# Kernel tuning notes

Hardware: AMD Instinct MI355X
Metric: run time of the kernel (lower is better)

## Reference

```python
import jax, jax.numpy as jnp
import numpy as np

N = 100_000      # nodes
E = 3_200_000    # edges
H = 32           # hidden_dim
L = 4            # num_layers
G = 1_000        # graphs in batch
F_IN = 1         # num_features
C = 2            # num_classes
BN_EPS = 1e-5


def setup_inputs() -> dict:
    key = jax.random.key(0)
    ks = jax.random.split(key, 8)
    s = 0.1  # param init scale
    x = jax.random.normal(ks[0], (N, F_IN), jnp.float32)
    edge_index = jax.random.randint(ks[1], (2, E), 0, N, dtype=jnp.int64)
    batch = jnp.sort(jax.random.randint(ks[2], (N,), 0, G, dtype=jnp.int64))
    return {
        "x": x,
        "edge_index": edge_index,
        "batch": batch,
        "W_enc": jax.random.normal(ks[3], (F_IN, H), jnp.float32) * s,
        "b_enc": jnp.zeros((H,), jnp.float32),
        "eps": jnp.zeros((L,), jnp.float32),           # GIN train_eps, init 0
        "W1": jax.random.normal(ks[4], (L, H, H), jnp.float32) * s,
        "b1": jnp.zeros((L, H), jnp.float32),
        "W2": jax.random.normal(ks[5], (L, H, H), jnp.float32) * s,
        "b2": jnp.zeros((L, H), jnp.float32),
        "gamma": jnp.ones((L, H), jnp.float32),
        "beta": jnp.zeros((L, H), jnp.float32),
        "W_cls": jax.random.normal(ks[6], (H, C), jnp.float32) * s,
        "b_cls": jnp.zeros((C,), jnp.float32),
    }


def reference(x, edge_index, batch, W_enc, b_enc, eps, W1, b1, W2, b2,
              gamma, beta, W_cls, b_cls):
    h = x @ W_enc + b_enc                      # [N, H] node encoder
    src, dst = edge_index[0], edge_index[1]    # message flow src -> dst
    for l in range(L):
        # GINConv: (1+eps)*x + sum_{j in N(i)} x_j
        agg = jax.ops.segment_sum(h[src], dst, num_segments=N)   # [N, H]
        z = (1.0 + eps[l]) * h + agg
        # 2-layer MLP
        z = jnp.maximum(z @ W1[l] + b1[l], 0.0) @ W2[l] + b2[l]
        # BatchNorm1d (training-mode batch statistics over nodes)
        mu = z.mean(axis=0)
        var = z.var(axis=0)
        z = gamma[l] * (z - mu) * jax.lax.rsqrt(var + BN_EPS) + beta[l]
        h = jnp.maximum(z, 0.0)                # ReLU (dropout = identity, eval)
    pooled = jax.ops.segment_sum(h, batch, num_segments=G)   # global_add_pool
    return pooled @ W_cls + b_cls              # [G, C]
```

## Files before the change

kernel.cpp:

```cpp
#include <hip/hip_runtime.h>

#define N_NODES 100000
#define N_EDGES 3200000
#define HD      32
#define NLAYERS 4
#define NGRAPHS 1000
#define BN_EPS  1e-5f
#define BSHIFT  9
#define NBUCK   ((N_NODES + 511) >> 9)
#define PCHUNK  8192
#define NPB     ((N_EDGES + PCHUNK - 1) / PCHUNK)
#define ENC_BLOCKS ((N_NODES * 8 + 255) / 256)

typedef _Float16 f16;
typedef _Float16 f16x8 __attribute__((ext_vector_type(8)));
typedef float    f32x4 __attribute__((ext_vector_type(4)));
typedef int      i32x4 __attribute__((ext_vector_type(4)));
typedef unsigned int  u32x2 __attribute__((ext_vector_type(2)));
typedef unsigned char uc4 __attribute__((ext_vector_type(4)));
typedef unsigned char uc8 __attribute__((ext_vector_type(8)));

__global__ __launch_bounds__(256) void k_encphist(
    const float* __restrict__ x, const float* __restrict__ W_enc,
    const float* __restrict__ b_enc, const int* __restrict__ ei,
    unsigned char* __restrict__ hq, float* __restrict__ stats,
    float* __restrict__ pooled, int* __restrict__ pcnt)
{
    __shared__ int hist[256];
    int bb = blockIdx.x, t = threadIdx.x;
    if (bb < NPB) {
        hist[t] = 0;
        __syncthreads();
        int base4 = bb * (PCHUNK / 4);
        int n4 = min(PCHUNK / 4, N_EDGES / 4 - base4);
        const i32x4* d4 = (const i32x4*)(ei + N_EDGES);
        for (int k = t; k < n4; k += 256) {
            i32x4 d = __builtin_nontemporal_load(d4 + base4 + k);
            atomicAdd(&hist[d.x >> BSHIFT], 1);
            atomicAdd(&hist[d.y >> BSHIFT], 1);
            atomicAdd(&hist[d.z >> BSHIFT], 1);
            atomicAdd(&hist[d.w >> BSHIFT], 1);
        }
        __syncthreads();
        pcnt[t * NPB + bb] = hist[t];
    } else {
        int gid = (bb - NPB) * 256 + t;
        if (gid < NLAYERS * 64)   stats[gid]  = 0.f;
        if (gid < NGRAPHS * HD)   pooled[gid] = 0.f;
        if (gid < N_NODES * 8) {
            int i = gid >> 3, c0 = (gid & 7) * 4;
            float xv = x[i];
            uc4 r;
            #pragma unroll
            for (int k = 0; k < 4; ++k) {
                float w = W_enc[c0 + k];
                float s = 5.5f * fabsf(w) / 127.f + 1e-8f;
                int q = (int)rintf(xv * w / s) + 128;
                q = max(0, min(255, q));
                r[k] = (unsigned char)q;
            }
            *(uc4*)(hq + i * 32 + c0) = r;
        }
    }
}

__global__ __launch_bounds__(512) void k_pscanA(int* __restrict__ pcnt,
                                                int* __restrict__ btot)
{
    __shared__ int sc[2][512];
    int t = threadIdx.x, b = blockIdx.x;
    int base = b * NPB;
    int v = (t < NPB) ? pcnt[base + t] : 0;
    int pp = 0;
    sc[0][t] = v;
    __syncthreads();
    for (int st = 1; st < 512; st <<= 1) {
        int x = sc[pp][t];
        if (t >= st) x += sc[pp][t - st];
        sc[pp ^ 1][t] = x;
        pp ^= 1;
        __syncthreads();
    }
    int incl = sc[pp][t];
    if (t < NPB) pcnt[base + t] = incl - v;
    if (t == NPB - 1) btot[b] = incl;
}

__global__ __launch_bounds__(256) void k_pscatter(const int* __restrict__ ei,
                                                  const int* __restrict__ pcnt,
                                                  const int* __restrict__ btot,
                                                  unsigned int* __restrict__ ebuf)
{
    __shared__ int sb[2][256];
    __shared__ int lcur[256];
    int t = threadIdx.x, blk = blockIdx.x;
    sb[0][t] = (t < NBUCK) ? btot[t] : 0;
    __syncthreads();
    int pp = 0;
    for (int st = 1; st < 256; st <<= 1) {
        int v = sb[pp][t];
        if (t >= st) v += sb[pp][t - st];
        sb[pp ^ 1][t] = v;
        pp ^= 1;
        __syncthreads();
    }
    int bexcl = (t == 0) ? 0 : sb[pp][t - 1];
    lcur[t] = pcnt[t * NPB + blk] + bexcl;
    __syncthreads();
    int base4 = blk * (PCHUNK / 4);
    int n4 = min(PCHUNK / 4, N_EDGES / 4 - base4);
    const i32x4* s4 = (const i32x4*)ei;
    const i32x4* d4 = (const i32x4*)(ei + N_EDGES);
    for (int k = t; k < n4; k += 256) {
        i32x4 s = __builtin_nontemporal_load(s4 + base4 + k);
        i32x4 d = __builtin_nontemporal_load(d4 + base4 + k);
        int pos;
        pos = atomicAdd(&lcur[d.x >> BSHIFT], 1);
        ebuf[pos] = ((unsigned)s.x << BSHIFT) | (unsigned)(d.x & 511);
        pos = atomicAdd(&lcur[d.y >> BSHIFT], 1);
        ebuf[pos] = ((unsigned)s.y << BSHIFT) | (unsigned)(d.y & 511);
        pos = atomicAdd(&lcur[d.z >> BSHIFT], 1);
        ebuf[pos] = ((unsigned)s.z << BSHIFT) | (unsigned)(d.z & 511);
        pos = atomicAdd(&lcur[d.w >> BSHIFT], 1);
        ebuf[pos] = ((unsigned)s.w << BSHIFT) | (unsigned)(d.w & 511);
    }
}

__global__ __launch_bounds__(512) void k_bfinal(const unsigned int* __restrict__ ebuf,
                                                const int* __restrict__ btot,
                                                int* __restrict__ off,
                                                int* __restrict__ csr)
{
    __shared__ int sb[2][256];
    __shared__ int cnt[512], scanbuf[2][512], cur[512];
    int tid = threadIdx.x, b = blockIdx.x;
    if (tid < 256) sb[0][tid] = (tid < NBUCK) ? btot[tid] : 0;
    __syncthreads();
    int pp = 0;
    for (int st = 1; st < 256; st <<= 1) {
        if (tid < 256) {
            int v = sb[pp][tid];
            if (tid >= st) v += sb[pp][tid - st];
            sb[pp ^ 1][tid] = v;
        }
        pp ^= 1;
        __syncthreads();
    }
    int base = (b == 0) ? 0 : sb[pp][b - 1];
    int nE = sb[pp][b] - base;
    if (b == NBUCK - 1 && tid == 0) off[N_NODES] = sb[pp][NBUCK - 1];
    cnt[tid] = 0;
    __syncthreads();
    for (int e = tid; e < nE; e += 512)
        atomicAdd(&cnt[ebuf[base + e] & 511], 1);
    __syncthreads();
    int p2 = 0;
    scanbuf[0][tid] = cnt[tid];
    __syncthreads();
    for (int st = 1; st < 512; st <<= 1) {
        int v = scanbuf[p2][tid];
        if (tid >= st) v += scanbuf[p2][tid - st];
        scanbuf[p2 ^ 1][tid] = v;
        p2 ^= 1;
        __syncthreads();
    }
    int excl = scanbuf[p2][tid] - cnt[tid];
    cur[tid] = excl;
    int gnode = (b << BSHIFT) + tid;
    if (gnode < N_NODES) off[gnode] = base + excl;
    __syncthreads();
    for (int e = tid; e < nE; e += 512) {
        unsigned int p = ebuf[base + e];
        int pos = atomicAdd(&cur[p & 511], 1);
        csr[base + pos] = (int)(p >> BSHIFT);
    }
}

__global__ __launch_bounds__(256) void k_agg(
    const unsigned char* __restrict__ hq, const int* __restrict__ off,
    const int* __restrict__ csr, const float* __restrict__ epsArr,
    const float* __restrict__ gamma, const float* __restrict__ beta,
    const float* __restrict__ W_enc, const float* __restrict__ b_enc,
    f16* __restrict__ z1, int layer)
{
    int tid = threadIdx.x;
    int unit = tid >> 2, li = tid & 3;
    int node = blockIdx.x * 64 + unit;
    if (node >= N_NODES) return;
    int co = li * 8;
    float dq_s[8], dq_o[8];
    if (layer == 0) {
        #pragma unroll
        for (int k = 0; k < 8; ++k) {
            int ch = co + k;
            float w = W_enc[ch];
            float s = 5.5f * fabsf(w) / 127.f + 1e-8f;
            dq_s[k] = s;
            dq_o[k] = b_enc[ch] - 128.f * s;
        }
    } else {
        #pragma unroll
        for (int k = 0; k < 8; ++k) {
            int ch = co + k;
            float g = gamma[(layer - 1) * 32 + ch];
            float bb = beta[(layer - 1) * 32 + ch];
            float vmax = fmaxf(bb + 5.5f * fabsf(g), 0.f);
            dq_s[k] = fmaxf(vmax, 1e-6f) / 255.f;
            dq_o[k] = 0.f;
        }
    }
    float oneEps = 1.f + epsArr[layer];
    const unsigned MASK = 0x00FF00FFu;

    int j = off[node], jend = off[node + 1];
    float deg = (float)(jend - j);
    unsigned a0 = 0, a1 = 0, a2 = 0, a3 = 0;
    auto accum = [&](u32x2 v) {
        a0 += v.x & MASK; a1 += (v.x >> 8) & MASK;
        a2 += v.y & MASK; a3 += (v.y >> 8) & MASK;
    };
    while (j < jend && (j & 3))
        accum(*(const u32x2*)(hq + csr[j++] * 32 + co));
    int n8 = (jend - j) >> 3;
    for (int it = 0; it < n8; ++it) {
        i32x4 q0 = __builtin_nontemporal_load((const i32x4*)(csr + j));
        i32x4 q1 = __builtin_nontemporal_load((const i32x4*)(csr + j + 4));
        u32x2 g0 = *(const u32x2*)(hq + q0.x * 32 + co);
        u32x2 g1 = *(const u32x2*)(hq + q0.y * 32 + co);
        u32x2 g2 = *(const u32x2*)(hq + q0.z * 32 + co);
        u32x2 g3 = *(const u32x2*)(hq + q0.w * 32 + co);
        u32x2 g4 = *(const u32x2*)(hq + q1.x * 32 + co);
        u32x2 g5 = *(const u32x2*)(hq + q1.y * 32 + co);
        u32x2 g6 = *(const u32x2*)(hq + q1.z * 32 + co);
        u32x2 g7 = *(const u32x2*)(hq + q1.w * 32 + co);
        accum(g0); accum(g1); accum(g2); accum(g3);
        accum(g4); accum(g5); accum(g6); accum(g7);
        j += 8;
    }
    if (jend - j >= 4) {
        i32x4 q0 = *(const i32x4*)(csr + j);
        accum(*(const u32x2*)(hq + q0.x * 32 + co));
        accum(*(const u32x2*)(hq + q0.y * 32 + co));
        accum(*(const u32x2*)(hq + q0.z * 32 + co));
        accum(*(const u32x2*)(hq + q0.w * 32 + co));
        j += 4;
    }
    while (j < jend)
        accum(*(const u32x2*)(hq + csr[j++] * 32 + co));

    u32x2 gs = *(const u32x2*)(hq + node * 32 + co);
    float F[8];
    F[0] = (float)(a0 & 0xFFFF); F[2] = (float)(a0 >> 16);
    F[1] = (float)(a1 & 0xFFFF); F[3] = (float)(a1 >> 16);
    F[4] = (float)(a2 & 0xFFFF); F[6] = (float)(a2 >> 16);
    F[5] = (float)(a3 & 0xFFFF); F[7] = (float)(a3 >> 16);
    float qs[8];
    #pragma unroll
    for (int k = 0; k < 4; ++k) {
        qs[k]     = (float)((gs.x >> (8 * k)) & 255u);
        qs[k + 4] = (float)((gs.y >> (8 * k)) & 255u);
    }
    float degE = deg + oneEps;
    f16x8 r;
    #pragma unroll
    for (int k = 0; k < 8; ++k) {
        float Fk = F[k] + oneEps * qs[k];
        r[k] = (f16)(fmaf(dq_s[k], Fk, dq_o[k] * degE));
    }
    *(f16x8*)(z1 + (size_t)node * 32 + co) = r;
}

__global__ __launch_bounds__(256) void k_mlp(
    const f16* __restrict__ z1, const float* __restrict__ W1,
    const float* __restrict__ b1, const float* __restrict__ W2,
    const float* __restrict__ b2, f16* __restrict__ z2out,
    float* __restrict__ stats, int layer)
{
    __shared__ float T[4][16 * 36];
    __shared__ float redS[4][32], redQ[4][32];
    int tid = threadIdx.x, wave = tid >> 6, lane = tid & 63;
    int col = lane & 15, quad = lane >> 4;
    const float* W1l = W1 + layer * 1024;
    const float* W2l = W2 + layer * 1024;
    f16x8 w1a, w1b, w2a, w2b;
    #pragma unroll
    for (int j = 0; j < 8; ++j) {
        int k = quad * 8 + j;
        w1a[j] = (f16)W1l[k * 32 + col];
        w1b[j] = (f16)W1l[k * 32 + col + 16];
        w2a[j] = (f16)W2l[k * 32 + col];
        w2b[j] = (f16)W2l[k * 32 + col + 16];
    }
    float b1a = b1[layer * 32 + col], b1b = b1[layer * 32 + col + 16];
    float b2a = b2[layer * 32 + col], b2b = b2[layer * 32 + col + 16];
    f32x4 bias1a = {b1a, b1a, b1a, b1a}, bias1b = {b1b, b1b, b1b, b1b};
    f32x4 bias2a = {b2a, b2a, b2a, b2a}, bias2b = {b2b, b2b, b2b, b2b};
    float* Tw = T[wave];

    const int NT = N_NODES / 16;
    int gw = blockIdx.x * 4 + wave, nw = gridDim.x * 4;
    float sA = 0.f, qA = 0.f, sB = 0.f, qB = 0.f;

    for (int tile = gw; tile < NT; tile += nw) {
        int nb = tile * 16;
        f16x8 a = *(const f16x8*)(z1 + (size_t)(nb + col) * 32 + quad * 8);
        f32x4 m0 = __builtin_amdgcn_mfma_f32_16x16x32_f16(a, w1a, bias1a, 0, 0, 0);
        f32x4 m1 = __builtin_amdgcn_mfma_f32_16x16x32_f16(a, w1b, bias1b, 0, 0, 0);
        #pragma unroll
        for (int r = 0; r < 4; ++r) {
            int row = quad * 4 + r;
            Tw[row * 36 + col]      = fmaxf(m0[r], 0.f);
            Tw[row * 36 + col + 16] = fmaxf(m1[r], 0.f);
        }
        f32x4 t0 = *(const f32x4*)(Tw + col * 36 + quad * 8);
        f32x4 t1 = *(const f32x4*)(Tw + col * 36 + quad * 8 + 4);
        f16x8 a2;
        #pragma unroll
        for (int k = 0; k < 4; ++k) { a2[k] = (f16)t0[k]; a2[k + 4] = (f16)t1[k]; }
        f32x4 z0 = __builtin_amdgcn_mfma_f32_16x16x32_f16(a2, w2a, bias2a, 0, 0, 0);
        f32x4 zb = __builtin_amdgcn_mfma_f32_16x16x32_f16(a2, w2b, bias2b, 0, 0, 0);
        #pragma unroll
        for (int r = 0; r < 4; ++r) {
            int node = nb + quad * 4 + r;
            z2out[node * 32 + col]      = (f16)z0[r];
            z2out[node * 32 + col + 16] = (f16)zb[r];
            sA += z0[r]; qA += z0[r] * z0[r];
            sB += zb[r]; qB += zb[r] * zb[r];
        }
    }

    sA += __shfl_xor(sA, 16); sA += __shfl_xor(sA, 32);
    qA += __shfl_xor(qA, 16); qA += __shfl_xor(qA, 32);
    sB += __shfl_xor(sB, 16); sB += __shfl_xor(sB, 32);
    qB += __shfl_xor(qB, 16); qB += __shfl_xor(qB, 32);
    if (lane < 16) {
        redS[wave][col] = sA; redS[wave][col + 16] = sB;
        redQ[wave][col] = qA; redQ[wave][col + 16] = qB;
    }
    __syncthreads();
    if (tid < 64) {
        int sel = tid >> 5, cc = tid & 31;
        float s = 0.f;
        #pragma unroll
        for (int w = 0; w < 4; ++w) s += sel ? redQ[w][cc] : redS[w][cc];
        atomicAdd(&stats[layer * 64 + sel * 32 + cc], s);
    }
}

__global__ __launch_bounds__(256) void k_quant(
    const f16* __restrict__ z2, const float* __restrict__ stats,
    const float* __restrict__ gamma, const float* __restrict__ beta,
    unsigned char* __restrict__ hq, int layer)
{
    int idx = blockIdx.x * 256 + threadIdx.x;
    if (idx >= N_NODES * 4) return;
    int c0 = (idx & 3) * 8;
    const float invN = 1.0f / (float)N_NODES;
    float bnsc[8], bnsh[8], inv_s[8];
    #pragma unroll
    for (int k = 0; k < 8; ++k) {
        int ch = c0 + k;
        float g = gamma[layer * 32 + ch], bb = beta[layer * 32 + ch];
        float mu  = stats[layer * 64 + ch] * invN;
        float var = stats[layer * 64 + 32 + ch] * invN - mu * mu;
        float sc = g * rsqrtf(var + BN_EPS);
        bnsc[k] = sc;
        bnsh[k] = bb - mu * sc;
        float vmax = fmaxf(bb + 5.5f * fabsf(g), 0.f);
        inv_s[k] = 255.f / fmaxf(vmax, 1e-6f);
    }
    f16x8 z = *(const f16x8*)(z2 + (size_t)idx * 8);
    uc8 r;
    #pragma unroll
    for (int k = 0; k < 8; ++k) {
        float v = fmaxf(fmaf((float)z[k], bnsc[k], bnsh[k]), 0.f);
        int q = (int)(fminf(v * inv_s[k], 255.f) + 0.5f);
        r[k] = (unsigned char)q;
    }
    __builtin_nontemporal_store(r, (uc8*)(hq + (size_t)idx * 8));
}

__global__ __launch_bounds__(256) void k_pool(const f16* __restrict__ z2,
                                              const int* __restrict__ batch,
                                              const float* __restrict__ stats,
                                              const float* __restrict__ gamma,
                                              const float* __restrict__ beta,
                                              float* __restrict__ pooled)
{
    int c = threadIdx.x & 31, slot = threadIdx.x >> 5;
    const float invN = 1.0f / (float)N_NODES;
    float mu  = stats[3 * 64 + c] * invN;
    float var = stats[3 * 64 + 32 + c] * invN - mu * mu;
    float sc = gamma[3 * 32 + c] * rsqrtf(var + BN_EPS);
    float sh = beta[3 * 32 + c] - mu * sc;
    int start = blockIdx.x * 256 + slot * 32;
    if (start >= N_NODES) return;
    int end = min(start + 32, N_NODES);
    int cur = batch[start]; float acc = 0.f;
    for (int i = start; i < end; ++i) {
        int g = batch[i];
        if (g != cur) { atomicAdd(&pooled[cur * HD + c], acc); acc = 0.f; cur = g; }
        acc += fmaxf(fmaf((float)z2[i * 32 + c], sc, sh), 0.f);
    }
    atomicAdd(&pooled[cur * HD + c], acc);
}

__global__ __launch_bounds__(256) void k_cls(const float* __restrict__ pooled,
                                             const float* __restrict__ Wc,
                                             const float* __restrict__ bc,
                                             float* __restrict__ out)
{
    int gid = blockIdx.x * 256 + threadIdx.x;
    if (gid >= NGRAPHS * 2) return;
    int g = gid >> 1, c = gid & 1;
    float s = bc[c];
    #pragma unroll
    for (int k = 0; k < 32; ++k) s = fmaf(pooled[g * 32 + k], Wc[k * 2 + c], s);
    out[gid] = s;
}

extern "C" void kernel_launch(void* const* d_in, const int* in_sizes, int n_in,
                              void* d_out, int out_size, void* d_ws, size_t ws_size,
                              hipStream_t stream)
{
    const float* x      = (const float*)d_in[0];
    const int*   ei     = (const int*)d_in[1];
    const int*   batch  = (const int*)d_in[2];
    const float* W_enc  = (const float*)d_in[3];
    const float* b_enc  = (const float*)d_in[4];
    const float* epsArr = (const float*)d_in[5];
    const float* W1     = (const float*)d_in[6];
    const float* b1     = (const float*)d_in[7];
    const float* W2     = (const float*)d_in[8];
    const float* b2     = (const float*)d_in[9];
    const float* gamma  = (const float*)d_in[10];
    const float* beta   = (const float*)d_in[11];
    const float* Wc     = (const float*)d_in[12];
    const float* bc     = (const float*)d_in[13];
    float* out = (float*)d_out;

    char* ws = (char*)d_ws;
    size_t o = 0;
    auto alloc = [&](size_t bytes) {
        char* p = ws + o;
        o += (bytes + 255) & ~(size_t)255;
        return p;
    };
    unsigned char* hq = (unsigned char*)alloc((size_t)N_NODES * 32);
    f16*   z1     = (f16*) alloc((size_t)N_NODES * 32 * 2);
    f16*   z2     = (f16*) alloc((size_t)N_NODES * 32 * 2);
    int*   csr    = (int*) alloc((size_t)N_EDGES * 4);
    unsigned int* ebuf = (unsigned int*)alloc((size_t)N_EDGES * 4);
    int*   offA   = (int*) alloc((size_t)(N_NODES + 1) * 4);
    int*   pcnt   = (int*) alloc((size_t)256 * NPB * 4);
    int*   btot   = (int*) alloc(1024);
    float* stats  = (float*)alloc(NLAYERS * 64 * 4);
    float* pooled = (float*)alloc((size_t)NGRAPHS * HD * 4);

    k_encphist<<<NPB + ENC_BLOCKS, 256, 0, stream>>>(x, W_enc, b_enc, ei, hq,
                                                     stats, pooled, pcnt);
    k_pscanA  <<<NBUCK, 512, 0, stream>>>(pcnt, btot);
    k_pscatter<<<NPB, 256, 0, stream>>>(ei, pcnt, btot, ebuf);
    k_bfinal  <<<NBUCK, 512, 0, stream>>>(ebuf, btot, offA, csr);

    for (int l = 0; l < NLAYERS; ++l) {
        k_agg<<<(N_NODES + 63) / 64, 256, 0, stream>>>(hq, offA, csr, epsArr,
                                                       gamma, beta, W_enc, b_enc,
                                                       z1, l);
        k_mlp<<<782, 256, 0, stream>>>(z1, W1, b1, W2, b2, z2, stats, l);
        if (l < NLAYERS - 1)
            k_quant<<<(N_NODES * 4 + 255) / 256, 256, 0, stream>>>(z2, stats,
                                                                   gamma, beta,
                                                                   hq, l);
    }
    k_pool<<<(N_NODES + 255) / 256, 256, 0, stream>>>(z2, batch, stats,
                                                      gamma, beta, pooled);
    k_cls <<<8, 256, 0, stream>>>(pooled, Wc, bc, out);
}
```

Before: 443.6 us.

## Fuse neighbor aggregation with MLP and aggregate raw scalar input in layer 0

Result: no change. 442.8 us (-0.2%).

```diff
diff --git a/kernel.cpp b/kernel.cpp
--- a/kernel.cpp
+++ b/kernel.cpp
@@ -10,20 +10,17 @@
 #define NBUCK   ((N_NODES + 511) >> 9)
 #define PCHUNK  8192
 #define NPB     ((N_EDGES + PCHUNK - 1) / PCHUNK)
-#define ENC_BLOCKS ((N_NODES * 8 + 255) / 256)
+#define ZBLOCKS ((NGRAPHS * HD + 255) / 256)
 
 typedef _Float16 f16;
 typedef _Float16 f16x8 __attribute__((ext_vector_type(8)));
 typedef float    f32x4 __attribute__((ext_vector_type(4)));
 typedef int      i32x4 __attribute__((ext_vector_type(4)));
 typedef unsigned int  u32x2 __attribute__((ext_vector_type(2)));
-typedef unsigned char uc4 __attribute__((ext_vector_type(4)));
 typedef unsigned char uc8 __attribute__((ext_vector_type(8)));
 
 __global__ __launch_bounds__(256) void k_encphist(
-    const float* __restrict__ x, const float* __restrict__ W_enc,
-    const float* __restrict__ b_enc, const int* __restrict__ ei,
-    unsigned char* __restrict__ hq, float* __restrict__ stats,
+    const int* __restrict__ ei, float* __restrict__ stats,
     float* __restrict__ pooled, int* __restrict__ pcnt)
 {
     __shared__ int hist[256];
@@ -47,20 +44,6 @@
         int gid = (bb - NPB) * 256 + t;
         if (gid < NLAYERS * 64)   stats[gid]  = 0.f;
         if (gid < NGRAPHS * HD)   pooled[gid] = 0.f;
-        if (gid < N_NODES * 8) {
-            int i = gid >> 3, c0 = (gid & 7) * 4;
-            float xv = x[i];
-            uc4 r;
-            #pragma unroll
-            for (int k = 0; k < 4; ++k) {
-                float w = W_enc[c0 + k];
-                float s = 5.5f * fabsf(w) / 127.f + 1e-8f;
-                int q = (int)rintf(xv * w / s) + 128;
-                q = max(0, min(255, q));
-                r[k] = (unsigned char)q;
-            }
-            *(uc4*)(hq + i * 32 + c0) = r;
-        }
     }
 }
 
@@ -176,141 +159,135 @@
     }
 }
 
-__global__ __launch_bounds__(256) void k_agg(
-    const unsigned char* __restrict__ hq, const int* __restrict__ off,
-    const int* __restrict__ csr, const float* __restrict__ epsArr,
-    const float* __restrict__ gamma, const float* __restrict__ beta,
-    const float* __restrict__ W_enc, const float* __restrict__ b_enc,
-    f16* __restrict__ z1, int layer)
-{
-    int tid = threadIdx.x;
-    int unit = tid >> 2, li = tid & 3;
-    int node = blockIdx.x * 64 + unit;
-    if (node >= N_NODES) return;
-    int co = li * 8;
-    float dq_s[8], dq_o[8];
-    if (layer == 0) {
-        #pragma unroll
-        for (int k = 0; k < 8; ++k) {
-            int ch = co + k;
-            float w = W_enc[ch];
-            float s = 5.5f * fabsf(w) / 127.f + 1e-8f;
-            dq_s[k] = s;
-            dq_o[k] = b_enc[ch] - 128.f * s;
-        }
-    } else {
-        #pragma unroll
-        for (int k = 0; k < 8; ++k) {
-            int ch = co + k;
-            float g = gamma[(layer - 1) * 32 + ch];
-            float bb = beta[(layer - 1) * 32 + ch];
-            float vmax = fmaxf(bb + 5.5f * fabsf(g), 0.f);
-            dq_s[k] = fmaxf(vmax, 1e-6f) / 255.f;
-            dq_o[k] = 0.f;
-        }
-    }
-    float oneEps = 1.f + epsArr[layer];
-    const unsigned MASK = 0x00FF00FFu;
-
-    int j = off[node], jend = off[node + 1];
-    float deg = (float)(jend - j);
-    unsigned a0 = 0, a1 = 0, a2 = 0, a3 = 0;
-    auto accum = [&](u32x2 v) {
-        a0 += v.x & MASK; a1 += (v.x >> 8) & MASK;
-        a2 += v.y & MASK; a3 += (v.y >> 8) & MASK;
-    };
-    while (j < jend && (j & 3))
-        accum(*(const u32x2*)(hq + csr[j++] * 32 + co));
-    int n8 = (jend - j) >> 3;
-    for (int it = 0; it < n8; ++it) {
-        i32x4 q0 = __builtin_nontemporal_load((const i32x4*)(csr + j));
-        i32x4 q1 = __builtin_nontemporal_load((const i32x4*)(csr + j + 4));
-        u32x2 g0 = *(const u32x2*)(hq + q0.x * 32 + co);
-        u32x2 g1 = *(const u32x2*)(hq + q0.y * 32 + co);
-        u32x2 g2 = *(const u32x2*)(hq + q0.z * 32 + co);
-        u32x2 g3 = *(const u32x2*)(hq + q0.w * 32 + co);
-        u32x2 g4 = *(const u32x2*)(hq + q1.x * 32 + co);
-        u32x2 g5 = *(const u32x2*)(hq + q1.y * 32 + co);
-        u32x2 g6 = *(const u32x2*)(hq + q1.z * 32 + co);
-        u32x2 g7 = *(const u32x2*)(hq + q1.w * 32 + co);
-        accum(g0); accum(g1); accum(g2); accum(g3);
-        accum(g4); accum(g5); accum(g6); accum(g7);
-        j += 8;
-    }
-    if (jend - j >= 4) {
-        i32x4 q0 = *(const i32x4*)(csr + j);
-        accum(*(const u32x2*)(hq + q0.x * 32 + co));
-        accum(*(const u32x2*)(hq + q0.y * 32 + co));
-        accum(*(const u32x2*)(hq + q0.z * 32 + co));
-        accum(*(const u32x2*)(hq + q0.w * 32 + co));
-        j += 4;
-    }
-    while (j < jend)
-        accum(*(const u32x2*)(hq + csr[j++] * 32 + co));
-
-    u32x2 gs = *(const u32x2*)(hq + node * 32 + co);
-    float F[8];
-    F[0] = (float)(a0 & 0xFFFF); F[2] = (float)(a0 >> 16);
-    F[1] = (float)(a1 & 0xFFFF); F[3] = (float)(a1 >> 16);
-    F[4] = (float)(a2 & 0xFFFF); F[6] = (float)(a2 >> 16);
-    F[5] = (float)(a3 & 0xFFFF); F[7] = (float)(a3 >> 16);
-    float qs[8];
-    #pragma unroll
-    for (int k = 0; k < 4; ++k) {
-        qs[k]     = (float)((gs.x >> (8 * k)) & 255u);
-        qs[k + 4] = (float)((gs.y >> (8 * k)) & 255u);
-    }
-    float degE = deg + oneEps;
-    f16x8 r;
-    #pragma unroll
-    for (int k = 0; k < 8; ++k) {
-        float Fk = F[k] + oneEps * qs[k];
-        r[k] = (f16)(fmaf(dq_s[k], Fk, dq_o[k] * degE));
-    }
-    *(f16x8*)(z1 + (size_t)node * 32 + co) = r;
-}
-
-__global__ __launch_bounds__(256) void k_mlp(
-    const f16* __restrict__ z1, const float* __restrict__ W1,
+__global__ __launch_bounds__(256) void k_fused(
+    const unsigned char* __restrict__ hq, const float* __restrict__ x,
+    const int* __restrict__ off, const int* __restrict__ csr,
+    const float* __restrict__ epsArr, const float* __restrict__ gamma,
+    const float* __restrict__ beta, const float* __restrict__ W_enc,
+    const float* __restrict__ b_enc, const float* __restrict__ W1,
     const float* __restrict__ b1, const float* __restrict__ W2,
     const float* __restrict__ b2, f16* __restrict__ z2out,
     float* __restrict__ stats, int layer)
 {
+    __shared__ f16 AT[4][16][5][8];
     __shared__ float T[4][16 * 36];
     __shared__ float redS[4][32], redQ[4][32];
     int tid = threadIdx.x, wave = tid >> 6, lane = tid & 63;
     int col = lane & 15, quad = lane >> 4;
-    const float* W1l = W1 + layer * 1024;
-    const float* W2l = W2 + layer * 1024;
-    f16x8 w1a, w1b, w2a, w2b;
+    int unit = tid >> 2, li = tid & 3, ul = unit & 15;
+    int node = blockIdx.x * 64 + unit;
+    bool valid = node < N_NODES;
+    int co = li * 8;
+
+    f16x8 r;
     #pragma unroll
-    for (int j = 0; j < 8; ++j) {
-        int k = quad * 8 + j;
-        w1a[j] = (f16)W1l[k * 32 + col];
-        w1b[j] = (f16)W1l[k * 32 + col + 16];
-        w2a[j] = (f16)W2l[k * 32 + col];
-        w2b[j] = (f16)W2l[k * 32 + col + 16];
-    }
-    float b1a = b1[layer * 32 + col], b1b = b1[layer * 32 + col + 16];
-    float b2a = b2[layer * 32 + col], b2b = b2[layer * 32 + col + 16];
-    f32x4 bias1a = {b1a, b1a, b1a, b1a}, bias1b = {b1b, b1b, b1b, b1b};
-    f32x4 bias2a = {b2a, b2a, b2a, b2a}, bias2b = {b2b, b2b, b2b, b2b};
-    float* Tw = T[wave];
-
-    const int NT = N_NODES / 16;
-    int gw = blockIdx.x * 4 + wave, nw = gridDim.x * 4;
+    for (int k = 0; k < 8; ++k) r[k] = (f16)0.f;
+
+    if (valid) {
+        if (layer == 0) {
+            int j0 = off[node], jend = off[node + 1];
+            float S = 0.f;
+            for (int j = j0 + li; j < jend; j += 4) S += x[csr[j]];
+            S += __shfl_xor(S, 1);
+            S += __shfl_xor(S, 2);
+            float oneEps = 1.f + epsArr[0];
+            float u  = oneEps * x[node] + S;
+            float dv = oneEps + (float)(jend - j0);
+            #pragma unroll
+            for (int k = 0; k < 8; ++k)
+                r[k] = (f16)(fmaf(u, W_enc[co + k], dv * b_enc[co + k]));
+        } else {
+            float dq_s[8];
+            #pragma unroll
+            for (int k = 0; k < 8; ++k) {
+                int ch = co + k;
+                float g  = gamma[(layer - 1) * 32 + ch];
+                float bb = beta[(layer - 1) * 32 + ch];
+                float vmax = fmaxf(bb + 5.5f * fabsf(g), 0.f);
+                dq_s[k] = fmaxf(vmax, 1e-6f) / 255.f;
+            }
+            float oneEps = 1.f + epsArr[layer];
+            const unsigned MASK = 0x00FF00FFu;
+            int j = off[node], jend = off[node + 1];
+            unsigned a0 = 0, a1 = 0, a2 = 0, a3 = 0;
+            auto accum = [&](u32x2 v) {
+                a0 += v.x & MASK; a1 += (v.x >> 8) & MASK;
+                a2 += v.y & MASK; a3 += (v.y >> 8) & MASK;
+            };
+            while (j < jend && (j & 3))
+                accum(*(const u32x2*)(hq + csr[j++] * 32 + co));
+            int n8 = (jend - j) >> 3;
+            for (int it = 0; it < n8; ++it) {
+                i32x4 q0 = __builtin_nontemporal_load((const i32x4*)(csr + j));
+                i32x4 q1 = __builtin_nontemporal_load((const i32x4*)(csr + j + 4));
+                u32x2 g0 = *(const u32x2*)(hq + q0.x * 32 + co);
+                u32x2 g1 = *(const u32x2*)(hq + q0.y * 32 + co);
+                u32x2 g2 = *(const u32x2*)(hq + q0.z * 32 + co);
+                u32x2 g3 = *(const u32x2*)(hq + q0.w * 32 + co);
+                u32x2 g4 = *(const u32x2*)(hq + q1.x * 32 + co);
+                u32x2 g5 = *(const u32x2*)(hq + q1.y * 32 + co);
+                u32x2 g6 = *(const u32x2*)(hq + q1.z * 32 + co);
+                u32x2 g7 = *(const u32x2*)(hq + q1.w * 32 + co);
+                accum(g0); accum(g1); accum(g2); accum(g3);
+                accum(g4); accum(g5); accum(g6); accum(g7);
+                j += 8;
+            }
+            if (jend - j >= 4) {
+                i32x4 q0 = *(const i32x4*)(csr + j);
+                accum(*(const u32x2*)(hq + q0.x * 32 + co));
+                accum(*(const u32x2*)(hq + q0.y * 32 + co));
+                accum(*(const u32x2*)(hq + q0.z * 32 + co));
+                accum(*(const u32x2*)(hq + q0.w * 32 + co));
+                j += 4;
+            }
+            while (j < jend)
+                accum(*(const u32x2*)(hq + csr[j++] * 32 + co));
+
+            u32x2 gs = *(const u32x2*)(hq + node * 32 + co);
+            float F[8];
+            F[0] = (float)(a0 & 0xFFFF); F[2] = (float)(a0 >> 16);
+            F[1] = (float)(a1 & 0xFFFF); F[3] = (float)(a1 >> 16);
+            F[4] = (float)(a2 & 0xFFFF); F[6] = (float)(a2 >> 16);
+            F[5] = (float)(a3 & 0xFFFF); F[7] = (float)(a3 >> 16);
+            #pragma unroll
+            for (int k = 0; k < 4; ++k) {
+                float qsl = (float)((gs.x >> (8 * k)) & 255u);
+                float qsh = (float)((gs.y >> (8 * k)) & 255u);
+                r[k]     = (f16)(dq_s[k]     * (F[k]     + oneEps * qsl));
+                r[k + 4] = (f16)(dq_s[k + 4] * (F[k + 4] + oneEps * qsh));
+            }
+        }
+    }
+
+    if (valid) *(f16x8*)&AT[wave][ul][li][0] = r;
+
     float sA = 0.f, qA = 0.f, sB = 0.f, qB = 0.f;
-
-    for (int tile = gw; tile < NT; tile += nw) {
-        int nb = tile * 16;
-        f16x8 a = *(const f16x8*)(z1 + (size_t)(nb + col) * 32 + quad * 8);
+    if (valid) {
+        f16x8 a = *(const f16x8*)&AT[wave][col][quad][0];
+        const float* W1l = W1 + layer * 1024;
+        const float* W2l = W2 + layer * 1024;
+        f16x8 w1a, w1b, w2a, w2b;
+        #pragma unroll
+        for (int jj = 0; jj < 8; ++jj) {
+            int k = quad * 8 + jj;
+            w1a[jj] = (f16)W1l[k * 32 + col];
+            w1b[jj] = (f16)W1l[k * 32 + col + 16];
+            w2a[jj] = (f16)W2l[k * 32 + col];
+            w2b[jj] = (f16)W2l[k * 32 + col + 16];
+        }
+        float b1a = b1[layer * 32 + col], b1b = b1[layer * 32 + col + 16];
+        float b2a = b2[layer * 32 + col], b2b = b2[layer * 32 + col + 16];
+        f32x4 bias1a = {b1a, b1a, b1a, b1a}, bias1b = {b1b, b1b, b1b, b1b};
+        f32x4 bias2a = {b2a, b2a, b2a, b2a}, bias2b = {b2b, b2b, b2b, b2b};
+        float* Tw = T[wave];
+
         f32x4 m0 = __builtin_amdgcn_mfma_f32_16x16x32_f16(a, w1a, bias1a, 0, 0, 0);
         f32x4 m1 = __builtin_amdgcn_mfma_f32_16x16x32_f16(a, w1b, bias1b, 0, 0, 0);
         #pragma unroll
-        for (int r = 0; r < 4; ++r) {
-            int row = quad * 4 + r;
-            Tw[row * 36 + col]      = fmaxf(m0[r], 0.f);
-            Tw[row * 36 + col + 16] = fmaxf(m1[r], 0.f);
+        for (int rr = 0; rr < 4; ++rr) {
+            int row = quad * 4 + rr;
+            Tw[row * 36 + col]      = fmaxf(m0[rr], 0.f);
+            Tw[row * 36 + col + 16] = fmaxf(m1[rr], 0.f);
         }
         f32x4 t0 = *(const f32x4*)(Tw + col * 36 + quad * 8);
         f32x4 t1 = *(const f32x4*)(Tw + col * 36 + quad * 8 + 4);
@@ -319,13 +296,14 @@
         for (int k = 0; k < 4; ++k) { a2[k] = (f16)t0[k]; a2[k + 4] = (f16)t1[k]; }
         f32x4 z0 = __builtin_amdgcn_mfma_f32_16x16x32_f16(a2, w2a, bias2a, 0, 0, 0);
         f32x4 zb = __builtin_amdgcn_mfma_f32_16x16x32_f16(a2, w2b, bias2b, 0, 0, 0);
+        int nb = blockIdx.x * 64 + wave * 16;
         #pragma unroll
-        for (int r = 0; r < 4; ++r) {
-            int node = nb + quad * 4 + r;
-            z2out[node * 32 + col]      = (f16)z0[r];
-            z2out[node * 32 + col + 16] = (f16)zb[r];
-            sA += z0[r]; qA += z0[r] * z0[r];
-            sB += zb[r]; qB += zb[r] * zb[r];
+        for (int rr = 0; rr < 4; ++rr) {
+            int n2 = nb + quad * 4 + rr;
+            z2out[n2 * 32 + col]      = (f16)z0[rr];
+            z2out[n2 * 32 + col + 16] = (f16)zb[rr];
+            sA += z0[rr]; qA += z0[rr] * z0[rr];
+            sB += zb[rr]; qB += zb[rr] * zb[rr];
         }
     }
 
@@ -447,7 +425,6 @@
         return p;
     };
     unsigned char* hq = (unsigned char*)alloc((size_t)N_NODES * 32);
-    f16*   z1     = (f16*) alloc((size_t)N_NODES * 32 * 2);
     f16*   z2     = (f16*) alloc((size_t)N_NODES * 32 * 2);
     int*   csr    = (int*) alloc((size_t)N_EDGES * 4);
     unsigned int* ebuf = (unsigned int*)alloc((size_t)N_EDGES * 4);
@@ -457,17 +434,15 @@
     float* stats  = (float*)alloc(NLAYERS * 64 * 4);
     float* pooled = (float*)alloc((size_t)NGRAPHS * HD * 4);
 
-    k_encphist<<<NPB + ENC_BLOCKS, 256, 0, stream>>>(x, W_enc, b_enc, ei, hq,
-                                                     stats, pooled, pcnt);
+    k_encphist<<<NPB + ZBLOCKS, 256, 0, stream>>>(ei, stats, pooled, pcnt);
     k_pscanA  <<<NBUCK, 512, 0, stream>>>(pcnt, btot);
     k_pscatter<<<NPB, 256, 0, stream>>>(ei, pcnt, btot, ebuf);
     k_bfinal  <<<NBUCK, 512, 0, stream>>>(ebuf, btot, offA, csr);
 
     for (int l = 0; l < NLAYERS; ++l) {
-        k_agg<<<(N_NODES + 63) / 64, 256, 0, stream>>>(hq, offA, csr, epsArr,
-                                                       gamma, beta, W_enc, b_enc,
-                                                       z1, l);
-        k_mlp<<<782, 256, 0, stream>>>(z1, W1, b1, W2, b2, z2, stats, l);
+        k_fused<<<(N_NODES + 63) / 64, 256, 0, stream>>>(
+            hq, x, offA, csr, epsArr, gamma, beta, W_enc, b_enc,
+            W1, b1, W2, b2, z2, stats, l);
         if (l < NLAYERS - 1)
             k_quant<<<(N_NODES * 4 + 255) / 256, 256, 0, stream>>>(z2, stats,
                                                                    gamma, beta,
```
